# Kernel optimization log

Measured on AMD Instinct MI355X. Metric: run time of the kernel, lower is better.

Reference implementation:

```python
import jax, jax.numpy as jnp
import numpy as np

L, B, D = 512, 4, 1024          # seq(atoms), batch, embed dim
H, DH = 16, 64                  # heads, head dim
FF = 4096                       # ffn hidden
HP = 32                         # encoder_pair_embed_dim
K = 256                         # pbc-expanded atoms


def _ln(x, g, b):
    m = x.mean(-1, keepdims=True)
    v = x.var(-1, keepdims=True)
    return (x - m) / jnp.sqrt(v + 1e-5) * g + b


def _rope(x, pos):
    # x: [S,B,H,DH], pos: [B,S]
    inv_freq = 1.0 / (10000.0 ** (jnp.arange(0, DH, 2, dtype=jnp.float32) / DH))
    ang = pos.astype(jnp.float32)[..., None] * inv_freq          # [B,S,DH/2]
    cos = jnp.cos(ang).transpose(1, 0, 2)[:, :, None, :]          # [S,B,1,DH/2]
    sin = jnp.sin(ang).transpose(1, 0, 2)[:, :, None, :]
    x1, x2 = jnp.split(x, 2, axis=-1)
    return jnp.concatenate([x1 * cos - x2 * sin, x1 * sin + x2 * cos], axis=-1)


def setup_inputs() -> dict:
    key = jax.random.key(0)
    ks = jax.random.split(key, 12)
    s = 0.02
    return dict(
        x=jax.random.normal(ks[0], (L, B, D), jnp.float32),
        x_pair=jax.random.normal(ks[1], (L, L + K, B, HP), jnp.float32),
        padding_mask=jnp.zeros((B, L), bool),
        expand_mask=jnp.zeros((B, K), bool),
        position_ids=jnp.tile(jnp.arange(L, dtype=jnp.int32)[None, :], (B, 1)),
        outcell_index=jax.random.randint(ks[2], (B, K), 0, L, dtype=jnp.int32),
        wq=jax.random.normal(ks[3], (D, D), jnp.float32) * s,
        wk=jax.random.normal(ks[4], (D, D), jnp.float32) * s,
        wv=jax.random.normal(ks[5], (D, D), jnp.float32) * s,
        wo=jax.random.normal(ks[6], (D, D), jnp.float32) * s,
        fc1=jax.random.normal(ks[7], (D, FF), jnp.float32) * s,
        fc2=jax.random.normal(ks[8], (FF, D), jnp.float32) * s,
        top_ln_g=jnp.ones((D,), jnp.float32), top_ln_b=jnp.zeros((D,), jnp.float32),
        mid_ln_g=jnp.ones((D,), jnp.float32), mid_ln_b=jnp.zeros((D,), jnp.float32),
        pair_ln_g=jnp.ones((D,), jnp.float32), pair_ln_b=jnp.zeros((D,), jnp.float32),
        pair_w1=jax.random.normal(ks[9], (D, 2 * HP), jnp.float32) * s,
        pair_w2=jax.random.normal(ks[10], (2 * HP, HP), jnp.float32) * s,
    )


def reference(x, x_pair, padding_mask, expand_mask, position_ids, outcell_index,
              wq, wk, wv, wo, fc1, fc2,
              top_ln_g, top_ln_b, mid_ln_g, mid_ln_b,
              pair_ln_g, pair_ln_b, pair_w1, pair_w2):
    barange = jnp.arange(B)
    # ---- self-attention block (pre-LN, RoPE, pbc-expanded keys/values) ----
    residual = x
    h = _ln(x, top_ln_g, top_ln_b)                               # [L,B,D]
    h_exp = h[outcell_index.T, barange[None, :], :]               # [K,B,D] gather along L per batch
    kv_src = jnp.concatenate([h, h_exp], axis=0)                  # [L+K,B,D]
    q = (h @ wq).reshape(L, B, H, DH)
    k = (kv_src @ wk).reshape(L + K, B, H, DH)
    v = (kv_src @ wv).reshape(L + K, B, H, DH)
    pos_exp = position_ids[barange[:, None], outcell_index]       # [B,K]
    pos_k = jnp.concatenate([position_ids, pos_exp], axis=1)      # [B,L+K]
    q = _rope(q, position_ids)
    k = _rope(k, pos_k)
    scores = jnp.einsum('lbhd,kbhd->bhlk', q, k) / np.sqrt(DH)    # [B,H,L,L+K]
    kp_mask = jnp.concatenate([padding_mask, expand_mask], axis=1)  # [B,L+K]
    scores = jnp.where(kp_mask[:, None, None, :], -1e9, scores)
    attn = jax.nn.softmax(scores, axis=-1)
    o = jnp.einsum('bhlk,kbhd->lbhd', attn, v).reshape(L, B, D) @ wo
    x = residual + o
    # ---- FFN block ----
    residual = x
    h = _ln(x, mid_ln_g, mid_ln_b)
    x = residual + jax.nn.gelu(h @ fc1, approximate=False) @ fc2
    # ---- pair outer product ----
    x_p_i = jax.nn.silu(_ln(x, pair_ln_g, pair_ln_b) @ pair_w1) @ pair_w2   # [L,B,HP]
    expand_x_p_i = x_p_i[outcell_index.T, barange[None, :], :]              # [K,B,HP]
    x_p_j = jnp.concatenate([x_p_i, expand_x_p_i], axis=0)                  # [L+K,B,HP]
    x_pair = x_pair + jnp.einsum('lbh,kbh->lkbh', x_p_i, x_p_j)             # [L,L+K,B,HP]
    return x, x_pair
```

## Files before the change

kernel.cpp:

```cpp
#include <hip/hip_runtime.h>
#include <math.h>


typedef __bf16 bf16x8 __attribute__((ext_vector_type(8)));
typedef float f32x4 __attribute__((ext_vector_type(4)));

__device__ __forceinline__ unsigned short f2bf(float f) {
  unsigned u = __float_as_uint(f);
  u = (u + 0x7fffu + ((u >> 16) & 1u)) >> 16;
  return (unsigned short)u;
}
__device__ __forceinline__ float bf2f(unsigned short s) {
  return __uint_as_float(((unsigned)s) << 16);
}

__device__ __forceinline__ void gload_lds16(const void* g, void* l) {
  __builtin_amdgcn_global_load_lds(
      (__attribute__((address_space(1))) void*)g,
      (__attribute__((address_space(3))) void*)l, 16, 0, 0);
}

__global__ __launch_bounds__(256) void prep_all(
    const float* __restrict__ wq, const float* __restrict__ wk, const float* __restrict__ wv,
    const float* __restrict__ wo, const float* __restrict__ fc1, const float* __restrict__ fc2,
    const float* __restrict__ x, const int* __restrict__ oc, const int* __restrict__ pos_ids,
    const float* __restrict__ tln_g, const float* __restrict__ tln_b,
    unsigned short* __restrict__ qkvT, unsigned short* __restrict__ woT,
    unsigned short* __restrict__ fc1T, unsigned short* __restrict__ fc2T,
    unsigned short* __restrict__ kvb, int* __restrict__ posk) {
  __shared__ float smem[64 * 33];
  const int id = blockIdx.x, t = threadIdx.x;

  if (id < 6144) {
    const float* W; unsigned short* WT; int Kd, Nd, n0, k0;
    if (id < 2048) {
      int which = id >> 9, lid = id & 511;
      W = which == 0 ? wq : (which == 1 ? wk : (which == 2 ? wv : wo));
      WT = which < 3 ? qkvT + (long)which * 1024 * 1024 : woT;
      Kd = 1024; Nd = 1024;
      k0 = (lid >> 5) * 64; n0 = (lid & 31) * 32;
    } else if (id < 4096) {
      int lid = id - 2048;
      W = fc1; WT = fc1T; Kd = 1024; Nd = 4096;
      k0 = (lid >> 7) * 64; n0 = (lid & 127) * 32;
    } else {
      int lid = id - 4096;
      W = fc2; WT = fc2T; Kd = 4096; Nd = 1024;
      k0 = (lid >> 5) * 64; n0 = (lid & 31) * 32;
    }
    const int tx = t & 31, ty = t >> 5;
#pragma unroll
    for (int j = 0; j < 64; j += 8)
      smem[(ty + j) * 33 + tx] = W[(long)(k0 + ty + j) * Nd + n0 + tx];
    __syncthreads();
#pragma unroll
    for (int i = 0; i < 32; i += 8) {
      ushort2 o;
      o.x = f2bf(smem[(2 * tx) * 33 + ty + i]);
      o.y = f2bf(smem[(2 * tx + 1) * 33 + ty + i]);
      *(ushort2*)&WT[(long)(n0 + ty + i) * Kd + k0 + 2 * tx] = o;
    }
  } else if (id < 9216) {
    const int rowIdx = id - 6144;
    int srow;
    if (rowIdx < 2048) {
      srow = rowIdx;
    } else {
      int j = (rowIdx - 2048) >> 2, b = rowIdx & 3;
      srow = oc[b * 256 + j] * 4 + b;
    }
    const float* xr = x + (long)srow * 1024;
    float v[4]; float s = 0.f, ss = 0.f;
#pragma unroll
    for (int i = 0; i < 4; i++) { v[i] = xr[t + 256 * i]; s += v[i]; ss += v[i] * v[i]; }
#pragma unroll
    for (int o = 32; o > 0; o >>= 1) { s += __shfl_down(s, o); ss += __shfl_down(ss, o); }
    const int wave = t >> 6, lane = t & 63;
    if (lane == 0) { smem[wave] = s; smem[4 + wave] = ss; }
    __syncthreads();
    s = smem[0] + smem[1] + smem[2] + smem[3];
    ss = smem[4] + smem[5] + smem[6] + smem[7];
    const float mean = s * (1.f / 1024.f);
    const float rstd = rsqrtf(ss * (1.f / 1024.f) - mean * mean + 1e-5f);
#pragma unroll
    for (int i = 0; i < 4; i++) {
      const int c = t + 256 * i;
      kvb[(long)rowIdx * 1024 + c] = f2bf((v[i] - mean) * rstd * tln_g[c] + tln_b[c]);
    }
  } else {
    int i = (id - 9216) * 256 + t;
    if (i < 3072) {
      int s = i >> 2, b = i & 3;
      posk[i] = (s < 512) ? pos_ids[b * 512 + s]
                          : pos_ids[b * 512 + oc[b * 256 + s - 512]];
    }
  }
}

__global__ __launch_bounds__(256) void red_ln(
    const float* __restrict__ p0, const float* __restrict__ p1,
    const float* __restrict__ R, float* __restrict__ Xout,
    const float* __restrict__ g, const float* __restrict__ bb,
    unsigned short* __restrict__ Y) {
  const int row = blockIdx.x, t = threadIdx.x;
  const long base = (long)row * 1024;
  float v[4]; float s = 0.f, ss = 0.f;
#pragma unroll
  for (int i = 0; i < 4; i++) {
    const int c = t + 256 * i;
    float val = p0[base + c] + p1[base + c] + R[base + c];
    Xout[base + c] = val;
    v[i] = val; s += val; ss += val * val;
  }
#pragma unroll
  for (int o = 32; o > 0; o >>= 1) { s += __shfl_down(s, o); ss += __shfl_down(ss, o); }
  __shared__ float red[8];
  const int wave = t >> 6, lane = t & 63;
  if (lane == 0) { red[wave] = s; red[4 + wave] = ss; }
  __syncthreads();
  s = red[0] + red[1] + red[2] + red[3];
  ss = red[4] + red[5] + red[6] + red[7];
  const float mean = s * (1.f / 1024.f);
  const float rstd = rsqrtf(ss * (1.f / 1024.f) - mean * mean + 1e-5f);
#pragma unroll
  for (int i = 0; i < 4; i++) {
    const int c = t + 256 * i;
    Y[base + c] = f2bf((v[i] - mean) * rstd * g[c] + bb[c]);
  }
}

__global__ __launch_bounds__(256) void red_ln_pair(
    const float* __restrict__ p0, const float* __restrict__ p1,
    const float* __restrict__ R, float* __restrict__ Xout,
    const float* __restrict__ g, const float* __restrict__ bb,
    const float* __restrict__ w1, const float* __restrict__ w2,
    float* __restrict__ xpi) {
  const int row = blockIdx.x, t = threadIdx.x;
  const long base = (long)row * 1024;
  __shared__ float lnrow[1024];
  __shared__ float red[8];
  __shared__ float red2[64][4];
  __shared__ float s1[64];
  float v[4]; float s = 0.f, ss = 0.f;
#pragma unroll
  for (int i = 0; i < 4; i++) {
    const int c = t + 256 * i;
    float val = p0[base + c] + p1[base + c] + R[base + c];
    Xout[base + c] = val;
    v[i] = val; s += val; ss += val * val;
  }
#pragma unroll
  for (int o = 32; o > 0; o >>= 1) { s += __shfl_down(s, o); ss += __shfl_down(ss, o); }
  const int wave = t >> 6, lane = t & 63;
  if (lane == 0) { red[wave] = s; red[4 + wave] = ss; }
  __syncthreads();
  s = red[0] + red[1] + red[2] + red[3];
  ss = red[4] + red[5] + red[6] + red[7];
  const float mean = s * (1.f / 1024.f);
  const float rstd = rsqrtf(ss * (1.f / 1024.f) - mean * mean + 1e-5f);
#pragma unroll
  for (int i = 0; i < 4; i++) {
    const int c = t + 256 * i;
    lnrow[c] = (v[i] - mean) * rstd * g[c] + bb[c];
  }
  __syncthreads();
  const int c = t & 63, qt = t >> 6;
  float acc = 0.f;
  for (int k = qt * 256; k < qt * 256 + 256; k++)
    acc += lnrow[k] * w1[k * 64 + c];
  red2[c][qt] = acc;
  __syncthreads();
  if (t < 64) {
    float vv = red2[t][0] + red2[t][1] + red2[t][2] + red2[t][3];
    s1[t] = vv / (1.f + __expf(-vv));
  }
  __syncthreads();
  if (t < 32) {
    float o = 0.f;
    for (int k = 0; k < 64; k++) o += s1[k] * w2[k * 32 + t];
    xpi[(long)row * 32 + t] = o;
  }
}

template <int EPI>
__global__ __launch_bounds__(256) void gemm_nt(
    const unsigned short* __restrict__ A, const unsigned short* __restrict__ BT,
    void* __restrict__ Cout, const float* __restrict__ R, int M, int N, int Kd) {
  __shared__ __align__(16) unsigned short As[128 * 32];
  __shared__ __align__(16) unsigned short Bs[128 * 32];
  const int t = threadIdx.x;
  const int wave = t >> 6, lane = t & 63;
  const int m0 = blockIdx.y * 128, n0 = blockIdx.x * 128;
  const int wr = wave >> 1, wc = wave & 1;
  const int lr = lane & 15, lg = lane >> 4;

  f32x4 acc[4][4] = {};

  const int srow = 32 * wave + (lane >> 2);
  const int schunk = (lane & 3) * 8;
  const unsigned short* Ag = A + (long)(m0 + srow) * Kd + schunk;
  const unsigned short* Bg = BT + (long)(n0 + srow) * Kd + schunk;
  unsigned short* AsW = &As[(32 * wave) * 32];
  unsigned short* BsW = &Bs[(32 * wave) * 32];

  for (int k0 = 0; k0 < Kd; k0 += 32) {
    __syncthreads();
    gload_lds16(Ag + k0, AsW);
    gload_lds16(Ag + k0 + 16 * (long)Kd, AsW + 16 * 32);
    gload_lds16(Bg + k0, BsW);
    gload_lds16(Bg + k0 + 16 * (long)Kd, BsW + 16 * 32);
    asm volatile("s_waitcnt vmcnt(0)" ::: "memory");
    __syncthreads();

    bf16x8 af[4], bfr[4];
#pragma unroll
    for (int mf = 0; mf < 4; mf++)
      af[mf] = *(const bf16x8*)&As[(64 * wr + 16 * mf + lr) * 32 + lg * 8];
#pragma unroll
    for (int nf = 0; nf < 4; nf++)
      bfr[nf] = *(const bf16x8*)&Bs[(64 * wc + 16 * nf + lr) * 32 + lg * 8];
#pragma unroll
    for (int mf = 0; mf < 4; mf++)
#pragma unroll
      for (int nf = 0; nf < 4; nf++)
        acc[mf][nf] = __builtin_amdgcn_mfma_f32_16x16x32_bf16(af[mf], bfr[nf], acc[mf][nf], 0, 0, 0);
  }

#pragma unroll
  for (int mf = 0; mf < 4; mf++)
#pragma unroll
    for (int nf = 0; nf < 4; nf++)
#pragma unroll
      for (int r = 0; r < 4; r++) {
        const int row = m0 + 64 * wr + 16 * mf + 4 * lg + r;
        const int col = n0 + 64 * wc + 16 * nf + lr;
        const long off = (long)row * N + col;
        float v = acc[mf][nf][r];
        if constexpr (EPI == 1) {
          ((float*)Cout)[off] = v + R[off];
        } else if constexpr (EPI == 2) {
          float gl = 0.5f * v * (1.0f + erff(v * 0.70710678118654752f));
          ((unsigned short*)Cout)[off] = f2bf(gl);
        } else if constexpr (EPI == 3) {
          ((unsigned short*)Cout)[off] = f2bf(v);
        } else {
          ((float*)Cout)[off] = v;
        }
      }
}

__global__ __launch_bounds__(256) void gemm_qkv(
    const unsigned short* __restrict__ A, const unsigned short* __restrict__ BT,
    unsigned short* __restrict__ Cout) {
  constexpr int N = 3072, Kd = 1024;
  int bid = blockIdx.x;
  int mt, nt;
  if (bid < 384) { mt = bid / 24; nt = bid % 24; }
  else { int rem = bid - 384; mt = 16 + (rem >> 4); nt = 8 + (rem & 15); }
  const int m0 = mt * 128, n0 = nt * 128;

  __shared__ __align__(16) unsigned short As[128 * 32];
  __shared__ __align__(16) unsigned short Bs[128 * 32];
  const int t = threadIdx.x;
  const int wave = t >> 6, lane = t & 63;
  const int wr = wave >> 1, wc = wave & 1;
  const int lr = lane & 15, lg = lane >> 4;

  f32x4 acc[4][4] = {};

  const int srow = 32 * wave + (lane >> 2);
  const int schunk = (lane & 3) * 8;
  const unsigned short* Ag = A + (long)(m0 + srow) * Kd + schunk;
  const unsigned short* Bg = BT + (long)(n0 + srow) * Kd + schunk;
  unsigned short* AsW = &As[(32 * wave) * 32];
  unsigned short* BsW = &Bs[(32 * wave) * 32];

  for (int k0 = 0; k0 < Kd; k0 += 32) {
    __syncthreads();
    gload_lds16(Ag + k0, AsW);
    gload_lds16(Ag + k0 + 16 * (long)Kd, AsW + 16 * 32);
    gload_lds16(Bg + k0, BsW);
    gload_lds16(Bg + k0 + 16 * (long)Kd, BsW + 16 * 32);
    asm volatile("s_waitcnt vmcnt(0)" ::: "memory");
    __syncthreads();

    bf16x8 af[4], bfr[4];
#pragma unroll
    for (int mf = 0; mf < 4; mf++)
      af[mf] = *(const bf16x8*)&As[(64 * wr + 16 * mf + lr) * 32 + lg * 8];
#pragma unroll
    for (int nf = 0; nf < 4; nf++)
      bfr[nf] = *(const bf16x8*)&Bs[(64 * wc + 16 * nf + lr) * 32 + lg * 8];
#pragma unroll
    for (int mf = 0; mf < 4; mf++)
#pragma unroll
      for (int nf = 0; nf < 4; nf++)
        acc[mf][nf] = __builtin_amdgcn_mfma_f32_16x16x32_bf16(af[mf], bfr[nf], acc[mf][nf], 0, 0, 0);
  }

#pragma unroll
  for (int mf = 0; mf < 4; mf++)
#pragma unroll
    for (int nf = 0; nf < 4; nf++)
#pragma unroll
      for (int r = 0; r < 4; r++) {
        const int row = m0 + 64 * wr + 16 * mf + 4 * lg + r;
        const int col = n0 + 64 * wc + 16 * nf + lr;
        Cout[(long)row * N + col] = f2bf(acc[mf][nf][r]);
      }
}

__global__ __launch_bounds__(256) void gemm_nt_splitk(
    const unsigned short* __restrict__ A, const unsigned short* __restrict__ BT,
    float* __restrict__ Cp, int M, int N, int Kd) {
  const int kh = Kd >> 1;
  const long kbase = (long)blockIdx.z * kh;
  const unsigned short* A2 = A + kbase;
  const unsigned short* B2 = BT + kbase;
  float* Cz = Cp + (long)blockIdx.z * M * N;

  __shared__ __align__(16) unsigned short As[128 * 32];
  __shared__ __align__(16) unsigned short Bs[128 * 32];
  const int t = threadIdx.x;
  const int wave = t >> 6, lane = t & 63;
  const int m0 = blockIdx.y * 128, n0 = blockIdx.x * 128;
  const int wr = wave >> 1, wc = wave & 1;
  const int lr = lane & 15, lg = lane >> 4;

  f32x4 acc[4][4] = {};

  const int srow = 32 * wave + (lane >> 2);
  const int schunk = (lane & 3) * 8;
  const unsigned short* Ag = A2 + (long)(m0 + srow) * Kd + schunk;
  const unsigned short* Bg = B2 + (long)(n0 + srow) * Kd + schunk;
  unsigned short* AsW = &As[(32 * wave) * 32];
  unsigned short* BsW = &Bs[(16 * wave) * 64];

  BsW = &Bs[(32 * wave) * 32];

  for (int k0 = 0; k0 < kh; k0 += 32) {
    __syncthreads();
    gload_lds16(Ag + k0, AsW);
    gload_lds16(Ag + k0 + 16 * (long)Kd, AsW + 16 * 32);
    gload_lds16(Bg + k0, BsW);
    gload_lds16(Bg + k0 + 16 * (long)Kd, BsW + 16 * 32);
    asm volatile("s_waitcnt vmcnt(0)" ::: "memory");
    __syncthreads();

    bf16x8 af[4], bfr[4];
#pragma unroll
    for (int mf = 0; mf < 4; mf++)
      af[mf] = *(const bf16x8*)&As[(64 * wr + 16 * mf + lr) * 32 + lg * 8];
#pragma unroll
    for (int nf = 0; nf < 4; nf++)
      bfr[nf] = *(const bf16x8*)&Bs[(64 * wc + 16 * nf + lr) * 32 + lg * 8];
#pragma unroll
    for (int mf = 0; mf < 4; mf++)
#pragma unroll
      for (int nf = 0; nf < 4; nf++)
        acc[mf][nf] = __builtin_amdgcn_mfma_f32_16x16x32_bf16(af[mf], bfr[nf], acc[mf][nf], 0, 0, 0);
  }

#pragma unroll
  for (int mf = 0; mf < 4; mf++)
#pragma unroll
    for (int nf = 0; nf < 4; nf++)
#pragma unroll
      for (int r = 0; r < 4; r++) {
        const int row = m0 + 64 * wr + 16 * mf + 4 * lg + r;
        const int col = n0 + 64 * wc + 16 * nf + lr;
        Cz[(long)row * N + col] = acc[mf][nf][r];
      }
}

__global__ __launch_bounds__(256) void rope_vt(
    const unsigned short* __restrict__ QKV, const int* __restrict__ posk,
    unsigned short* __restrict__ qb, unsigned short* __restrict__ kbh,
    unsigned short* __restrict__ vth) {
  const int bid = blockIdx.x, t = threadIdx.x;
  if (bid < 10240) {
    int idx = bid * 256 + t;
    bool isq = idx < 1048576;
    int rp = isq ? idx : idx - 1048576;
    int p = rp & 511;
    int row = rp >> 9;
    int hh = p >> 5, dp = p & 31;
    int s = row >> 2, b = row & 3;
    int pos = isq ? posk[s * 4 + b] : posk[s * 4 + b + (s < 512 ? 0 : 0)];
    if (!isq) pos = posk[s * 4 + b];
    const unsigned short* src = QKV + (long)row * 3072 + (isq ? 0 : 1024) + hh * 64 + dp;
    float x1 = bf2f(src[0]), x2 = bf2f(src[32]);
    float invf = exp2f((float)dp * -0.41524101186091903f);
    float ang = (float)pos * invf;
    float sn = sinf(ang), cs = cosf(ang);
    float o1 = x1 * cs - x2 * sn, o2 = x1 * sn + x2 * cs;
    if (isq) {
      unsigned short* dst = qb + ((long)(b * 16 + hh) * 512 + s) * 64 + dp;
      dst[0] = f2bf(o1 * 0.125f); dst[32] = f2bf(o2 * 0.125f);
    } else {
      unsigned short* dst = kbh + ((long)(b * 16 + hh) * 768 + s) * 64 + dp;
      dst[0] = f2bf(o1); dst[32] = f2bf(o2);
    }
  } else {
    __shared__ unsigned short tile[64][72];
    const int vb = bid - 10240;
    const int kt = vb % 12, bh = vb / 12;
    const int b = bh >> 4, h = bh & 15;
    const int key = t >> 2, c = t & 3;
    const unsigned short* src =
        QKV + ((long)(kt * 64 + key) * 4 + b) * 3072 + 2048 + h * 64 + c * 16;
#pragma unroll
    for (int j = 0; j < 16; j++) tile[c * 16 + j][key] = src[j];
    __syncthreads();
    const int d = t >> 2;
    unsigned short* dst = vth + ((long)bh * 64 + d) * 768 + kt * 64 + c * 16;
    *(uint4*)dst = *(const uint4*)&tile[d][c * 16];
    *(uint4*)(dst + 8) = *(const uint4*)&tile[d][c * 16 + 8];
  }
}

__global__ __launch_bounds__(512) void att_mfma(
    const unsigned short* __restrict__ qb, const unsigned short* __restrict__ kbh,
    const unsigned short* __restrict__ vth,
    const unsigned char* __restrict__ pad_mask, const unsigned char* __restrict__ exp_mask,
    unsigned short* __restrict__ o_bf) {
  const int bh = blockIdx.y, b = bh >> 4, h = bh & 15;
  const int q0 = blockIdx.x * 128;
  const int t = threadIdx.x, wave = t >> 6, lane = t & 63;
  const int lr = lane & 15, lg = lane >> 4;

  __shared__ __align__(16) unsigned short Ps[8][16][72];
  __shared__ float maskAdd[768];

  for (int i = t; i < 768; i += 512)
    maskAdd[i] = ((i < 512) ? pad_mask[b * 512 + i] : exp_mask[b * 256 + i - 512]) ? -1e9f : 0.f;

  const unsigned short* qrow = qb + ((long)bh * 512 + q0 + wave * 16 + lr) * 64;
  const bf16x8 aq0 = *(const bf16x8*)(qrow + lg * 8);
  const bf16x8 aq1 = *(const bf16x8*)(qrow + 32 + lg * 8);
  __syncthreads();

  float m_run[4] = {-1e30f, -1e30f, -1e30f, -1e30f};
  float l_run[4] = {0.f, 0.f, 0.f, 0.f};
  f32x4 Oacc[4] = {};

  const unsigned short* kb0 = kbh + (long)bh * 768 * 64;
  const unsigned short* vb0 = vth + (long)bh * 64 * 768;

  for (int kt = 0; kt < 12; ++kt) {
    float sv[4][4];
#pragma unroll
    for (int nf = 0; nf < 4; nf++) {
      const unsigned short* kr = kb0 + (long)(kt * 64 + nf * 16 + lr) * 64;
      f32x4 z = {};
      bf16x8 b0 = *(const bf16x8*)(kr + lg * 8);
      bf16x8 b1 = *(const bf16x8*)(kr + 32 + lg * 8);
      z = __builtin_amdgcn_mfma_f32_16x16x32_bf16(aq0, b0, z, 0, 0, 0);
      z = __builtin_amdgcn_mfma_f32_16x16x32_bf16(aq1, b1, z, 0, 0, 0);
      float ma = maskAdd[kt * 64 + nf * 16 + lr];
#pragma unroll
      for (int r = 0; r < 4; r++) sv[nf][r] = z[r] + ma;
    }
    float mnew[4], scale[4], rs[4];
#pragma unroll
    for (int r = 0; r < 4; r++) {
      float tm = fmaxf(fmaxf(sv[0][r], sv[1][r]), fmaxf(sv[2][r], sv[3][r]));
      tm = fmaxf(tm, __shfl_xor(tm, 1));
      tm = fmaxf(tm, __shfl_xor(tm, 2));
      tm = fmaxf(tm, __shfl_xor(tm, 4));
      tm = fmaxf(tm, __shfl_xor(tm, 8));
      mnew[r] = fmaxf(m_run[r], tm);
      scale[r] = __expf(m_run[r] - mnew[r]);
      m_run[r] = mnew[r];
      rs[r] = 0.f;
    }
#pragma unroll
    for (int nf = 0; nf < 4; nf++)
#pragma unroll
      for (int r = 0; r < 4; r++) {
        float p = __expf(sv[nf][r] - mnew[r]);
        rs[r] += p;
        Ps[wave][lg * 4 + r][nf * 16 + lr] = f2bf(p);
      }
#pragma unroll
    for (int r = 0; r < 4; r++) {
      float x = rs[r];
      x += __shfl_xor(x, 1); x += __shfl_xor(x, 2);
      x += __shfl_xor(x, 4); x += __shfl_xor(x, 8);
      l_run[r] = l_run[r] * scale[r] + x;
#pragma unroll
      for (int nf = 0; nf < 4; nf++) Oacc[nf][r] *= scale[r];
    }
    bf16x8 ap0 = *(const bf16x8*)&Ps[wave][lr][lg * 8];
    bf16x8 ap1 = *(const bf16x8*)&Ps[wave][lr][32 + lg * 8];
#pragma unroll
    for (int nf = 0; nf < 4; nf++) {
      const unsigned short* vr = vb0 + (long)(nf * 16 + lr) * 768 + kt * 64;
      bf16x8 b0 = *(const bf16x8*)(vr + lg * 8);
      bf16x8 b1 = *(const bf16x8*)(vr + 32 + lg * 8);
      Oacc[nf] = __builtin_amdgcn_mfma_f32_16x16x32_bf16(ap0, b0, Oacc[nf], 0, 0, 0);
      Oacc[nf] = __builtin_amdgcn_mfma_f32_16x16x32_bf16(ap1, b1, Oacc[nf], 0, 0, 0);
    }
  }

#pragma unroll
  for (int r = 0; r < 4; r++) {
    float inv = 1.0f / l_run[r];
    int l = q0 + wave * 16 + lg * 4 + r;
#pragma unroll
    for (int nf = 0; nf < 4; nf++)
      o_bf[(((long)l * 4 + b) * 16 + h) * 64 + nf * 16 + lr] = f2bf(Oacc[nf][r] * inv);
  }
}

__global__ __launch_bounds__(256) void pair_update(
    const float* __restrict__ x_pair, const float* __restrict__ xpi,
    const int* __restrict__ oc, float* __restrict__ out) {
  int idx4 = blockIdx.x * 256 + threadIdx.x;
  int h4 = idx4 & 7;
  int lkb = idx4 >> 3;
  int b = lkb & 3;
  int lk = lkb >> 2;
  int kk = lk % 768;
  int l = lk / 768;
  int src = (kk < 512) ? kk : oc[b * 256 + kk - 512];
  float4 pv = ((const float4*)x_pair)[idx4];
  float4 a = ((const float4*)xpi)[(l * 4 + b) * 8 + h4];
  float4 bb = ((const float4*)xpi)[(src * 4 + b) * 8 + h4];
  float4 o;
  o.x = pv.x + a.x * bb.x; o.y = pv.y + a.y * bb.y;
  o.z = pv.z + a.z * bb.z; o.w = pv.w + a.w * bb.w;
  ((float4*)out)[idx4] = o;
}

extern "C" void kernel_launch(void* const* d_in, const int* in_sizes, int n_in,
                              void* d_out, int out_size, void* d_ws, size_t ws_size,
                              hipStream_t stream) {
  const float* x        = (const float*)d_in[0];
  const float* x_pair   = (const float*)d_in[1];
  const unsigned char* pad_mask = (const unsigned char*)d_in[2];
  const unsigned char* exp_mask = (const unsigned char*)d_in[3];
  const int* pos_ids    = (const int*)d_in[4];
  const int* oc         = (const int*)d_in[5];
  const float* wq  = (const float*)d_in[6];
  const float* wk  = (const float*)d_in[7];
  const float* wv  = (const float*)d_in[8];
  const float* wo  = (const float*)d_in[9];
  const float* fc1 = (const float*)d_in[10];
  const float* fc2 = (const float*)d_in[11];
  const float* tln_g = (const float*)d_in[12];
  const float* tln_b = (const float*)d_in[13];
  const float* mln_g = (const float*)d_in[14];
  const float* mln_b = (const float*)d_in[15];
  const float* pln_g = (const float*)d_in[16];
  const float* pln_b = (const float*)d_in[17];
  const float* w1 = (const float*)d_in[18];
  const float* w2 = (const float*)d_in[19];

  char* wsp = (char*)d_ws;
  size_t off = 0;
  auto alloc = [&](size_t bytes) -> void* {
    void* p = wsp + off;
    off = (off + bytes + 255) & ~(size_t)255;
    return p;
  };
  unsigned short* qkvT = (unsigned short*)alloc(3072LL * 1024 * 2);
  unsigned short* woT  = (unsigned short*)alloc(1024LL * 1024 * 2);
  unsigned short* fc1T = (unsigned short*)alloc(4096LL * 1024 * 2);
  unsigned short* fc2T = (unsigned short*)alloc(1024LL * 4096 * 2);
  unsigned short* kvb  = (unsigned short*)alloc(3072LL * 1024 * 2);
  int* posk            = (int*)alloc(3072LL * 4);
  unsigned short* QKVb = (unsigned short*)alloc(3072LL * 3072 * 2);
  unsigned short* qb   = (unsigned short*)alloc(64LL * 512 * 64 * 2);
  unsigned short* kbh  = (unsigned short*)alloc(64LL * 768 * 64 * 2);
  unsigned short* vth  = (unsigned short*)alloc(64LL * 64 * 768 * 2);
  unsigned short* obf  = (unsigned short*)alloc(2048LL * 1024 * 2);
  float* x1            = (float*)alloc(2048LL * 1024 * 4);
  unsigned short* h2   = (unsigned short*)alloc(2048LL * 1024 * 2);
  unsigned short* gbf  = (unsigned short*)alloc(2048LL * 4096 * 2);
  float* xpi           = (float*)alloc(2048LL * 32 * 4);
  float* pp            = (float*)alloc(2LL * 2048 * 1024 * 4);
  (void)ws_size; (void)in_sizes; (void)n_in; (void)out_size;

  prep_all<<<9228, 256, 0, stream>>>(wq, wk, wv, wo, fc1, fc2, x, oc, pos_ids,
                                     tln_g, tln_b, qkvT, woT, fc1T, fc2T, kvb, posk);

  gemm_qkv<<<512, 256, 0, stream>>>(kvb, qkvT, QKVb);

  rope_vt<<<11008, 256, 0, stream>>>(QKVb, posk, qb, kbh, vth);

  att_mfma<<<dim3(4, 64), 512, 0, stream>>>(qb, kbh, vth, pad_mask, exp_mask, obf);

  gemm_nt_splitk<<<dim3(8, 16, 2), 256, 0, stream>>>(obf, woT, pp, 2048, 1024, 1024);
  red_ln<<<2048, 256, 0, stream>>>(pp, pp + 2097152, x, x1, mln_g, mln_b, h2);

  gemm_nt<2><<<dim3(32, 16), 256, 0, stream>>>(h2, fc1T, gbf, nullptr, 2048, 4096, 1024);

  gemm_nt_splitk<<<dim3(8, 16, 2), 256, 0, stream>>>(gbf, fc2T, pp, 2048, 1024, 4096);
  red_ln_pair<<<2048, 256, 0, stream>>>(pp, pp + 2097152, x1, (float*)d_out,
                                        pln_g, pln_b, w1, w2, xpi);

  pair_update<<<49152, 256, 0, stream>>>(x_pair, xpi, oc, (float*)d_out + 2097152);
}
```

Measured before the change: 311.1 us.

## Vectorize LayerNorm and RoPE memory access, grid-stride pair update

The three LayerNorm paths now load and store four contiguous elements per thread with float4/ushort4 accesses instead of strided scalar loops. The RoPE kernel handles two adjacent dimensions per thread with paired loads and stores and uses fast __sincosf, which halves its block count. The pair update kernel becomes a grid-stride loop over 2048 blocks instead of 49152. Together these target memory-transaction count and launch overhead, at the cost of slightly lower sin/cos accuracy.

```diff
diff --git a/kernel.cpp b/kernel.cpp
--- a/kernel.cpp
+++ b/kernel.cpp
@@ -69,10 +69,9 @@
       int j = (rowIdx - 2048) >> 2, b = rowIdx & 3;
       srow = oc[b * 256 + j] * 4 + b;
     }
-    const float* xr = x + (long)srow * 1024;
-    float v[4]; float s = 0.f, ss = 0.f;
-#pragma unroll
-    for (int i = 0; i < 4; i++) { v[i] = xr[t + 256 * i]; s += v[i]; ss += v[i] * v[i]; }
+    const float4 vv = *(const float4*)(x + (long)srow * 1024 + t * 4);
+    float s = vv.x + vv.y + vv.z + vv.w;
+    float ss = vv.x * vv.x + vv.y * vv.y + vv.z * vv.z + vv.w * vv.w;
 #pragma unroll
     for (int o = 32; o > 0; o >>= 1) { s += __shfl_down(s, o); ss += __shfl_down(ss, o); }
     const int wave = t >> 6, lane = t & 63;
@@ -82,11 +81,14 @@
     ss = smem[4] + smem[5] + smem[6] + smem[7];
     const float mean = s * (1.f / 1024.f);
     const float rstd = rsqrtf(ss * (1.f / 1024.f) - mean * mean + 1e-5f);
-#pragma unroll
-    for (int i = 0; i < 4; i++) {
-      const int c = t + 256 * i;
-      kvb[(long)rowIdx * 1024 + c] = f2bf((v[i] - mean) * rstd * tln_g[c] + tln_b[c]);
-    }
+    const float4 gg = *(const float4*)(tln_g + t * 4);
+    const float4 bbv = *(const float4*)(tln_b + t * 4);
+    ushort4 o;
+    o.x = f2bf((vv.x - mean) * rstd * gg.x + bbv.x);
+    o.y = f2bf((vv.y - mean) * rstd * gg.y + bbv.y);
+    o.z = f2bf((vv.z - mean) * rstd * gg.z + bbv.z);
+    o.w = f2bf((vv.w - mean) * rstd * gg.w + bbv.w);
+    *(ushort4*)&kvb[(long)rowIdx * 1024 + t * 4] = o;
   } else {
     int i = (id - 9216) * 256 + t;
     if (i < 3072) {
@@ -103,15 +105,16 @@
     const float* __restrict__ g, const float* __restrict__ bb,
     unsigned short* __restrict__ Y) {
   const int row = blockIdx.x, t = threadIdx.x;
-  const long base = (long)row * 1024;
-  float v[4]; float s = 0.f, ss = 0.f;
-#pragma unroll
-  for (int i = 0; i < 4; i++) {
-    const int c = t + 256 * i;
-    float val = p0[base + c] + p1[base + c] + R[base + c];
-    Xout[base + c] = val;
-    v[i] = val; s += val; ss += val * val;
-  }
+  const long base4 = (long)row * 256 + t;
+  const float4 a = ((const float4*)p0)[base4];
+  const float4 b4 = ((const float4*)p1)[base4];
+  const float4 r4 = ((const float4*)R)[base4];
+  float4 v;
+  v.x = a.x + b4.x + r4.x; v.y = a.y + b4.y + r4.y;
+  v.z = a.z + b4.z + r4.z; v.w = a.w + b4.w + r4.w;
+  ((float4*)Xout)[base4] = v;
+  float s = v.x + v.y + v.z + v.w;
+  float ss = v.x * v.x + v.y * v.y + v.z * v.z + v.w * v.w;
 #pragma unroll
   for (int o = 32; o > 0; o >>= 1) { s += __shfl_down(s, o); ss += __shfl_down(ss, o); }
   __shared__ float red[8];
@@ -122,11 +125,14 @@
   ss = red[4] + red[5] + red[6] + red[7];
   const float mean = s * (1.f / 1024.f);
   const float rstd = rsqrtf(ss * (1.f / 1024.f) - mean * mean + 1e-5f);
-#pragma unroll
-  for (int i = 0; i < 4; i++) {
-    const int c = t + 256 * i;
-    Y[base + c] = f2bf((v[i] - mean) * rstd * g[c] + bb[c]);
-  }
+  const float4 gg = *(const float4*)(g + t * 4);
+  const float4 bbv = *(const float4*)(bb + t * 4);
+  ushort4 o;
+  o.x = f2bf((v.x - mean) * rstd * gg.x + bbv.x);
+  o.y = f2bf((v.y - mean) * rstd * gg.y + bbv.y);
+  o.z = f2bf((v.z - mean) * rstd * gg.z + bbv.z);
+  o.w = f2bf((v.w - mean) * rstd * gg.w + bbv.w);
+  ((ushort4*)Y)[base4] = o;
 }
 
 __global__ __launch_bounds__(256) void red_ln_pair(
@@ -136,19 +142,20 @@
     const float* __restrict__ w1, const float* __restrict__ w2,
     float* __restrict__ xpi) {
   const int row = blockIdx.x, t = threadIdx.x;
-  const long base = (long)row * 1024;
+  const long base4 = (long)row * 256 + t;
   __shared__ float lnrow[1024];
   __shared__ float red[8];
   __shared__ float red2[64][4];
   __shared__ float s1[64];
-  float v[4]; float s = 0.f, ss = 0.f;
-#pragma unroll
-  for (int i = 0; i < 4; i++) {
-    const int c = t + 256 * i;
-    float val = p0[base + c] + p1[base + c] + R[base + c];
-    Xout[base + c] = val;
-    v[i] = val; s += val; ss += val * val;
-  }
+  const float4 a = ((const float4*)p0)[base4];
+  const float4 b4 = ((const float4*)p1)[base4];
+  const float4 r4 = ((const float4*)R)[base4];
+  float4 v;
+  v.x = a.x + b4.x + r4.x; v.y = a.y + b4.y + r4.y;
+  v.z = a.z + b4.z + r4.z; v.w = a.w + b4.w + r4.w;
+  ((float4*)Xout)[base4] = v;
+  float s = v.x + v.y + v.z + v.w;
+  float ss = v.x * v.x + v.y * v.y + v.z * v.z + v.w * v.w;
 #pragma unroll
   for (int o = 32; o > 0; o >>= 1) { s += __shfl_down(s, o); ss += __shfl_down(ss, o); }
   const int wave = t >> 6, lane = t & 63;
@@ -158,11 +165,14 @@
   ss = red[4] + red[5] + red[6] + red[7];
   const float mean = s * (1.f / 1024.f);
   const float rstd = rsqrtf(ss * (1.f / 1024.f) - mean * mean + 1e-5f);
-#pragma unroll
-  for (int i = 0; i < 4; i++) {
-    const int c = t + 256 * i;
-    lnrow[c] = (v[i] - mean) * rstd * g[c] + bb[c];
-  }
+  const float4 gg = *(const float4*)(g + t * 4);
+  const float4 bbv = *(const float4*)(bb + t * 4);
+  float4 ln;
+  ln.x = (v.x - mean) * rstd * gg.x + bbv.x;
+  ln.y = (v.y - mean) * rstd * gg.y + bbv.y;
+  ln.z = (v.z - mean) * rstd * gg.z + bbv.z;
+  ln.w = (v.w - mean) * rstd * gg.w + bbv.w;
+  *(float4*)&lnrow[t * 4] = ln;
   __syncthreads();
   const int c = t & 63, qt = t >> 6;
   float acc = 0.f;
@@ -334,9 +344,7 @@
   const unsigned short* Ag = A2 + (long)(m0 + srow) * Kd + schunk;
   const unsigned short* Bg = B2 + (long)(n0 + srow) * Kd + schunk;
   unsigned short* AsW = &As[(32 * wave) * 32];
-  unsigned short* BsW = &Bs[(16 * wave) * 64];
-
-  BsW = &Bs[(32 * wave) * 32];
+  unsigned short* BsW = &Bs[(32 * wave) * 32];
 
   for (int k0 = 0; k0 < kh; k0 += 32) {
     __syncthreads();
@@ -378,32 +386,39 @@
     unsigned short* __restrict__ qb, unsigned short* __restrict__ kbh,
     unsigned short* __restrict__ vth) {
   const int bid = blockIdx.x, t = threadIdx.x;
-  if (bid < 10240) {
+  if (bid < 5120) {
     int idx = bid * 256 + t;
-    bool isq = idx < 1048576;
-    int rp = isq ? idx : idx - 1048576;
-    int p = rp & 511;
-    int row = rp >> 9;
-    int hh = p >> 5, dp = p & 31;
+    bool isq = idx < 524288;
+    int rp = isq ? idx : idx - 524288;
+    int p = rp & 255;
+    int row = rp >> 8;
+    int hh = p >> 4, dpp = (p & 15) * 2;
     int s = row >> 2, b = row & 3;
-    int pos = isq ? posk[s * 4 + b] : posk[s * 4 + b + (s < 512 ? 0 : 0)];
-    if (!isq) pos = posk[s * 4 + b];
-    const unsigned short* src = QKV + (long)row * 3072 + (isq ? 0 : 1024) + hh * 64 + dp;
-    float x1 = bf2f(src[0]), x2 = bf2f(src[32]);
-    float invf = exp2f((float)dp * -0.41524101186091903f);
-    float ang = (float)pos * invf;
-    float sn = sinf(ang), cs = cosf(ang);
-    float o1 = x1 * cs - x2 * sn, o2 = x1 * sn + x2 * cs;
-    if (isq) {
-      unsigned short* dst = qb + ((long)(b * 16 + hh) * 512 + s) * 64 + dp;
-      dst[0] = f2bf(o1 * 0.125f); dst[32] = f2bf(o2 * 0.125f);
-    } else {
-      unsigned short* dst = kbh + ((long)(b * 16 + hh) * 768 + s) * 64 + dp;
-      dst[0] = f2bf(o1); dst[32] = f2bf(o2);
-    }
+    int pos = posk[s * 4 + b];
+    const unsigned short* src = QKV + (long)row * 3072 + (isq ? 0 : 1024) + hh * 64 + dpp;
+    ushort2 xa = *(const ushort2*)src;
+    ushort2 xb = *(const ushort2*)(src + 32);
+    const float cfr = 0.41524101186091903f;
+    float i0 = exp2f(-(float)dpp * cfr);
+    float i1 = exp2f(-(float)(dpp + 1) * cfr);
+    float s0, c0, s1, c1;
+    __sincosf((float)pos * i0, &s0, &c0);
+    __sincosf((float)pos * i1, &s1, &c1);
+    float x1a = bf2f(xa.x), x1b = bf2f(xa.y);
+    float x2a = bf2f(xb.x), x2b = bf2f(xb.y);
+    float qs = isq ? 0.125f : 1.0f;
+    ushort2 o1, o2;
+    o1.x = f2bf((x1a * c0 - x2a * s0) * qs);
+    o1.y = f2bf((x1b * c1 - x2b * s1) * qs);
+    o2.x = f2bf((x1a * s0 + x2a * c0) * qs);
+    o2.y = f2bf((x1b * s1 + x2b * c1) * qs);
+    unsigned short* dst = (isq ? qb + ((long)(b * 16 + hh) * 512 + s) * 64
+                               : kbh + ((long)(b * 16 + hh) * 768 + s) * 64) + dpp;
+    *(ushort2*)dst = o1;
+    *(ushort2*)(dst + 32) = o2;
   } else {
     __shared__ unsigned short tile[64][72];
-    const int vb = bid - 10240;
+    const int vb = bid - 5120;
     const int kt = vb % 12, bh = vb / 12;
     const int b = bh >> 4, h = bh & 15;
     const int key = t >> 2, c = t & 3;
@@ -516,21 +531,22 @@
 __global__ __launch_bounds__(256) void pair_update(
     const float* __restrict__ x_pair, const float* __restrict__ xpi,
     const int* __restrict__ oc, float* __restrict__ out) {
-  int idx4 = blockIdx.x * 256 + threadIdx.x;
-  int h4 = idx4 & 7;
-  int lkb = idx4 >> 3;
-  int b = lkb & 3;
-  int lk = lkb >> 2;
-  int kk = lk % 768;
-  int l = lk / 768;
-  int src = (kk < 512) ? kk : oc[b * 256 + kk - 512];
-  float4 pv = ((const float4*)x_pair)[idx4];
-  float4 a = ((const float4*)xpi)[(l * 4 + b) * 8 + h4];
-  float4 bb = ((const float4*)xpi)[(src * 4 + b) * 8 + h4];
-  float4 o;
-  o.x = pv.x + a.x * bb.x; o.y = pv.y + a.y * bb.y;
-  o.z = pv.z + a.z * bb.z; o.w = pv.w + a.w * bb.w;
-  ((float4*)out)[idx4] = o;
+  for (int idx4 = blockIdx.x * 256 + threadIdx.x; idx4 < 12582912; idx4 += 2048 * 256) {
+    int h4 = idx4 & 7;
+    int lkb = idx4 >> 3;
+    int b = lkb & 3;
+    int lk = lkb >> 2;
+    int kk = lk % 768;
+    int l = lk / 768;
+    int src = (kk < 512) ? kk : oc[b * 256 + kk - 512];
+    float4 pv = ((const float4*)x_pair)[idx4];
+    float4 a = ((const float4*)xpi)[(l * 4 + b) * 8 + h4];
+    float4 bb = ((const float4*)xpi)[(src * 4 + b) * 8 + h4];
+    float4 o;
+    o.x = pv.x + a.x * bb.x; o.y = pv.y + a.y * bb.y;
+    o.z = pv.z + a.z * bb.z; o.w = pv.w + a.w * bb.w;
+    ((float4*)out)[idx4] = o;
+  }
 }
 
 extern "C" void kernel_launch(void* const* d_in, const int* in_sizes, int n_in,
@@ -587,7 +603,7 @@
 
   gemm_qkv<<<512, 256, 0, stream>>>(kvb, qkvT, QKVb);
 
-  rope_vt<<<11008, 256, 0, stream>>>(QKVb, posk, qb, kbh, vth);
+  rope_vt<<<5888, 256, 0, stream>>>(QKVb, posk, qb, kbh, vth);
 
   att_mfma<<<dim3(4, 64), 512, 0, stream>>>(qb, kbh, vth, pad_mask, exp_mask, obf);
 
@@ -600,5 +616,5 @@
   red_ln_pair<<<2048, 256, 0, stream>>>(pp, pp + 2097152, x1, (float*)d_out,
                                         pln_g, pln_b, w1, w2, xpi);
 
-  pair_update<<<49152, 256, 0, stream>>>(x_pair, xpi, oc, (float*)d_out + 2097152);
-}
+  pair_update<<<2048, 256, 0, stream>>>(x_pair, xpi, oc, (float*)d_out + 2097152);
+}
```

Result: slower. 321.2 us (+3.2%).
